# Kernel tuning notes

Measured on AMD Instinct MI355X. Metric: run time of the kernel, lower is better.

## Reference

```python
import jax, jax.numpy as jnp
import numpy as np

B, C, H, W = 32, 1, 720, 1280


def setup_inputs() -> dict:
    key = jax.random.key(0)
    k1, k2 = jax.random.split(key)
    right_img = jax.random.normal(k1, (B, C, H, W), dtype=jnp.float32)
    # disparity in [0, 64): realistic stereo disparities, some pixels sample out of bounds
    disp = jax.random.uniform(k2, (B, C, H, W), dtype=jnp.float32) * 64.0
    return {"right_img": right_img, "disp": disp}


def _warp(right_img, disp):
    b, c, h, w = right_img.shape
    dt = disp.dtype
    # grid construction (align_corners=True style normalization, as in the module)
    xs = jnp.arange(w, dtype=dt)  # [W]
    ys = jnp.arange(h, dtype=dt)  # [H]
    gx = xs[None, None, :] - disp[:, 0]                      # [B,H,W]
    gx = (gx - (w - 1) / 2) / (w - 1) * 2
    gy = (ys[None, :, None] - (h - 1) / 2) / (h - 1) * 2     # [1,H,1]
    gy = jnp.broadcast_to(gy, gx.shape)                      # [B,H,W]
    # F.grid_sample default: bilinear, align_corners=False, padding_mode='zeros'
    ix = ((gx + 1) * w - 1) / 2
    iy = ((gy + 1) * h - 1) / 2
    x0 = jnp.floor(ix)
    y0 = jnp.floor(iy)
    wx1 = ix - x0
    wy1 = iy - y0
    wx0 = 1.0 - wx1
    wy0 = 1.0 - wy1
    x0i = x0.astype(jnp.int32)
    y0i = y0.astype(jnp.int32)
    x1i = x0i + 1
    y1i = y0i + 1

    def gather(img, yy, xx):  # img [C,H,W]; yy,xx [H,W] -> [C,H,W]
        valid = (xx >= 0) & (xx < w) & (yy >= 0) & (yy < h)
        xc = jnp.clip(xx, 0, w - 1)
        yc = jnp.clip(yy, 0, h - 1)
        return img[:, yc, xc] * valid[None].astype(img.dtype)

    g = jax.vmap(gather)
    v00 = g(right_img, y0i, x0i)
    v01 = g(right_img, y0i, x1i)
    v10 = g(right_img, y1i, x0i)
    v11 = g(right_img, y1i, x1i)
    out = (v00 * (wy0 * wx0)[:, None] + v01 * (wy0 * wx1)[:, None]
           + v10 * (wy1 * wx0)[:, None] + v11 * (wy1 * wx1)[:, None])
    return out  # [B,C,H,W]


def reference(right_img, disp):
    return _warp(right_img, disp)
```

## Files before the change

### kernel.cpp

```cpp
#include <hip/hip_runtime.h>

constexpr int Bn = 32;
constexpr int Hn = 720;
constexpr int Wn = 1280;

__global__ __launch_bounds__(320) void warp_kernel(
    const float* __restrict__ img,
    const float* __restrict__ disp,
    float* __restrict__ out)
{
    __shared__ float srow[2 * Wn];

    const int hw  = Hn * Wn;
    const int blk = blockIdx.x;
    const int b   = blk / Hn;
    const int y   = blk - b * Hn;
    const int tid = threadIdx.x;

    float gy  = (((float)y - (float)(Hn - 1) * 0.5f) / (float)(Hn - 1)) * 2.0f;
    float iy  = ((gy + 1.0f) * (float)Hn - 1.0f) * 0.5f;
    float fy0 = floorf(iy);
    float wy1 = iy - fy0;
    float wy0 = 1.0f - wy1;
    int   y0  = (int)fy0;
    int   y1  = y0 + 1;
    bool  vy0 = (y0 >= 0) && (y0 < Hn);
    bool  vy1 = (y1 >= 0) && (y1 < Hn);
    int   y0c = min(max(y0, 0), Hn - 1);
    int   y1c = min(max(y1, 0), Hn - 1);

    const float* __restrict__ imb = img + (long long)b * hw;

    {
        const float4* __restrict__ src0 = reinterpret_cast<const float4*>(imb + (long long)y0c * Wn);
        const float4* __restrict__ src1 = reinterpret_cast<const float4*>(imb + (long long)y1c * Wn);
        float4* dst = reinterpret_cast<float4*>(srow);
        dst[tid]       = src0[tid];
        dst[320 + tid] = src1[tid];
    }
    __syncthreads();

    const float* __restrict__ r0 = srow;
    const float* __restrict__ r1 = srow + Wn;

    const long long base = (long long)blk * Wn + 4 * tid;
    const float4 d4 = *reinterpret_cast<const float4*>(disp + base);
    float dv[4] = {d4.x, d4.y, d4.z, d4.w};
    float res[4];

    const float my0 = vy0 ? 1.0f : 0.0f;
    const float my1 = vy1 ? 1.0f : 0.0f;

#pragma unroll
    for (int i = 0; i < 4; ++i) {
        float xf  = (float)(4 * tid + i);
        float gx  = ((xf - dv[i] - (float)(Wn - 1) * 0.5f) / (float)(Wn - 1)) * 2.0f;
        float ix  = ((gx + 1.0f) * (float)Wn - 1.0f) * 0.5f;
        float fx0 = floorf(ix);
        float wx1 = ix - fx0;
        float wx0 = 1.0f - wx1;
        int   x0  = (int)fx0;
        int   x1  = x0 + 1;
        float mx0 = ((x0 >= 0) && (x0 < Wn)) ? 1.0f : 0.0f;
        float mx1 = ((x1 >= 0) && (x1 < Wn)) ? 1.0f : 0.0f;
        int   x0c = min(max(x0, 0), Wn - 1);
        int   x1c = min(max(x1, 0), Wn - 1);

        float v00 = r0[x0c] * (my0 * mx0);
        float v01 = r0[x1c] * (my0 * mx1);
        float v10 = r1[x0c] * (my1 * mx0);
        float v11 = r1[x1c] * (my1 * mx1);

        res[i] = v00 * (wy0 * wx0) + v01 * (wy0 * wx1)
               + v10 * (wy1 * wx0) + v11 * (wy1 * wx1);
    }

    float4 o4 = make_float4(res[0], res[1], res[2], res[3]);
    *reinterpret_cast<float4*>(out + base) = o4;
}

extern "C" void kernel_launch(void* const* d_in, const int* in_sizes, int n_in,
                              void* d_out, int out_size, void* d_ws, size_t ws_size,
                              hipStream_t stream) {
    const float* img  = (const float*)d_in[0];
    const float* disp = (const float*)d_in[1];
    float* out = (float*)d_out;

    const int grid  = Bn * Hn;
    const int block = 320;

    warp_kernel<<<grid, block, 0, stream>>>(img, disp, out);
}
```

Baseline: 271.5 us.

## Process eight output rows per block sharing staged source rows in LDS

Each block now handles an 8-row tile of one image. It stages only the distinct source rows needed (about 9-10) into shared memory, instead of loading two rows per output row. Each wavefront computes one output row over five float4 chunks. This cuts redundant image reads and the number of blocks. In exchange, LDS use per block is larger, which may reduce occupancy, and load/compute overlap within a block is lost.

```diff
diff --git a/kernel.cpp b/kernel.cpp
--- a/kernel.cpp
+++ b/kernel.cpp
@@ -3,80 +3,102 @@
 constexpr int Bn = 32;
 constexpr int Hn = 720;
 constexpr int Wn = 1280;
+constexpr int RY = 8;
+constexpr int MAXR = RY + 2;
 
-__global__ __launch_bounds__(320) void warp_kernel(
+__device__ __forceinline__ void vcoord(int y, int& y0, float& wy1) {
+    float gy  = (((float)y - (float)(Hn - 1) * 0.5f) / (float)(Hn - 1)) * 2.0f;
+    float iy  = ((gy + 1.0f) * (float)Hn - 1.0f) * 0.5f;
+    float fy0 = floorf(iy);
+    wy1 = iy - fy0;
+    y0  = (int)fy0;
+}
+
+__global__ __launch_bounds__(512) void warp_kernel(
     const float* __restrict__ img,
     const float* __restrict__ disp,
     float* __restrict__ out)
 {
-    __shared__ float srow[2 * Wn];
+    __shared__ float srow[MAXR * Wn];
 
-    const int hw  = Hn * Wn;
-    const int blk = blockIdx.x;
-    const int b   = blk / Hn;
-    const int y   = blk - b * Hn;
-    const int tid = threadIdx.x;
+    const int hw   = Hn * Wn;
+    const int tile = blockIdx.x;
+    const int b    = tile / (Hn / RY);
+    const int Y    = (tile - b * (Hn / RY)) * RY;
+    const int tid  = threadIdx.x;
 
-    float gy  = (((float)y - (float)(Hn - 1) * 0.5f) / (float)(Hn - 1)) * 2.0f;
-    float iy  = ((gy + 1.0f) * (float)Hn - 1.0f) * 0.5f;
-    float fy0 = floorf(iy);
-    float wy1 = iy - fy0;
-    float wy0 = 1.0f - wy1;
-    int   y0  = (int)fy0;
-    int   y1  = y0 + 1;
-    bool  vy0 = (y0 >= 0) && (y0 < Hn);
-    bool  vy1 = (y1 >= 0) && (y1 < Hn);
-    int   y0c = min(max(y0, 0), Hn - 1);
-    int   y1c = min(max(y1, 0), Hn - 1);
+    int y0_first, y0_last; float dum;
+    vcoord(Y, y0_first, dum);
+    vcoord(Y + RY - 1, y0_last, dum);
+    const int lo = min(max(y0_first, 0), Hn - 1);
+    const int hi = min(max(y0_last + 1, 0), Hn - 1);
+    const int nr = hi - lo + 1;
 
     const float* __restrict__ imb = img + (long long)b * hw;
 
     {
-        const float4* __restrict__ src0 = reinterpret_cast<const float4*>(imb + (long long)y0c * Wn);
-        const float4* __restrict__ src1 = reinterpret_cast<const float4*>(imb + (long long)y1c * Wn);
+        const int nchunk = nr * (Wn / 4);
         float4* dst = reinterpret_cast<float4*>(srow);
-        dst[tid]       = src0[tid];
-        dst[320 + tid] = src1[tid];
+        for (int j = tid; j < nchunk; j += 512) {
+            int r  = j / (Wn / 4);
+            int cx = j - r * (Wn / 4);
+            dst[j] = reinterpret_cast<const float4*>(imb + (long long)(lo + r) * Wn)[cx];
+        }
     }
     __syncthreads();
 
-    const float* __restrict__ r0 = srow;
-    const float* __restrict__ r1 = srow + Wn;
+    const int w    = tid >> 6;
+    const int lane = tid & 63;
+    const int y    = Y + w;
 
-    const long long base = (long long)blk * Wn + 4 * tid;
-    const float4 d4 = *reinterpret_cast<const float4*>(disp + base);
-    float dv[4] = {d4.x, d4.y, d4.z, d4.w};
-    float res[4];
+    int y0; float wy1;
+    vcoord(y, y0, wy1);
+    const float wy0 = 1.0f - wy1;
+    const int   y1  = y0 + 1;
+    const float my0 = ((y0 >= 0) && (y0 < Hn)) ? 1.0f : 0.0f;
+    const float my1 = ((y1 >= 0) && (y1 < Hn)) ? 1.0f : 0.0f;
+    const int   y0c = min(max(y0, 0), Hn - 1);
+    const int   y1c = min(max(y1, 0), Hn - 1);
 
-    const float my0 = vy0 ? 1.0f : 0.0f;
-    const float my1 = vy1 ? 1.0f : 0.0f;
+    const float* __restrict__ r0 = srow + (y0c - lo) * Wn;
+    const float* __restrict__ r1 = srow + (y1c - lo) * Wn;
+
+    const long long rowbase = (long long)(b * Hn + y) * Wn;
 
 #pragma unroll
-    for (int i = 0; i < 4; ++i) {
-        float xf  = (float)(4 * tid + i);
-        float gx  = ((xf - dv[i] - (float)(Wn - 1) * 0.5f) / (float)(Wn - 1)) * 2.0f;
-        float ix  = ((gx + 1.0f) * (float)Wn - 1.0f) * 0.5f;
-        float fx0 = floorf(ix);
-        float wx1 = ix - fx0;
-        float wx0 = 1.0f - wx1;
-        int   x0  = (int)fx0;
-        int   x1  = x0 + 1;
-        float mx0 = ((x0 >= 0) && (x0 < Wn)) ? 1.0f : 0.0f;
-        float mx1 = ((x1 >= 0) && (x1 < Wn)) ? 1.0f : 0.0f;
-        int   x0c = min(max(x0, 0), Wn - 1);
-        int   x1c = min(max(x1, 0), Wn - 1);
+    for (int k = 0; k < 5; ++k) {
+        const int xpix = 4 * (lane + 64 * k);
+        const float4 d4 = *reinterpret_cast<const float4*>(disp + rowbase + xpix);
+        float dv[4] = {d4.x, d4.y, d4.z, d4.w};
+        float res[4];
 
-        float v00 = r0[x0c] * (my0 * mx0);
-        float v01 = r0[x1c] * (my0 * mx1);
-        float v10 = r1[x0c] * (my1 * mx0);
-        float v11 = r1[x1c] * (my1 * mx1);
+#pragma unroll
+        for (int i = 0; i < 4; ++i) {
+            float xf  = (float)(xpix + i);
+            float gx  = ((xf - dv[i] - (float)(Wn - 1) * 0.5f) / (float)(Wn - 1)) * 2.0f;
+            float ix  = ((gx + 1.0f) * (float)Wn - 1.0f) * 0.5f;
+            float fx0 = floorf(ix);
+            float wx1 = ix - fx0;
+            float wx0 = 1.0f - wx1;
+            int   x0  = (int)fx0;
+            int   x1  = x0 + 1;
+            float mx0 = ((x0 >= 0) && (x0 < Wn)) ? 1.0f : 0.0f;
+            float mx1 = ((x1 >= 0) && (x1 < Wn)) ? 1.0f : 0.0f;
+            int   x0c = min(max(x0, 0), Wn - 1);
+            int   x1c = min(max(x1, 0), Wn - 1);
 
-        res[i] = v00 * (wy0 * wx0) + v01 * (wy0 * wx1)
-               + v10 * (wy1 * wx0) + v11 * (wy1 * wx1);
+            float v00 = r0[x0c] * (my0 * mx0);
+            float v01 = r0[x1c] * (my0 * mx1);
+            float v10 = r1[x0c] * (my1 * mx0);
+            float v11 = r1[x1c] * (my1 * mx1);
+
+            res[i] = v00 * (wy0 * wx0) + v01 * (wy0 * wx1)
+                   + v10 * (wy1 * wx0) + v11 * (wy1 * wx1);
+        }
+
+        float4 o4 = make_float4(res[0], res[1], res[2], res[3]);
+        *reinterpret_cast<float4*>(out + rowbase + xpix) = o4;
     }
-
-    float4 o4 = make_float4(res[0], res[1], res[2], res[3]);
-    *reinterpret_cast<float4*>(out + base) = o4;
 }
 
 extern "C" void kernel_launch(void* const* d_in, const int* in_sizes, int n_in,
@@ -86,8 +108,8 @@
     const float* disp = (const float*)d_in[1];
     float* out = (float*)d_out;
 
-    const int grid  = Bn * Hn;
-    const int block = 320;
+    const int grid  = Bn * (Hn / RY);
+    const int block = 512;
 
     warp_kernel<<<grid, block, 0, stream>>>(img, disp, out);
 }
```

Result: slower. 279.4 us (+2.9%).
